# Performance work log

Hardware: AMD Instinct MI355X
Metric: run time of the kernel (lower is better)

The kernel has to match this reference:

```python
import jax, jax.numpy as jnp
import numpy as np

NUM_HEADS = 16

def setup_inputs() -> dict:
    key = jax.random.key(0)
    k1, k2, k3, k4, k5 = jax.random.split(key, 5)
    B, N, C = 4, 2048, 1024
    N2, Cy = 1024, 768
    x = jax.random.normal(k1, (B, N, C), dtype=jnp.float32)
    y = jax.random.normal(k2, (B, N2, Cy), dtype=jnp.float32)
    pad_mask = jax.random.randint(k3, (B, N), 0, 2).astype(jnp.bool_)
    # Linear weights (torch convention: out = inp @ W.T), scaled ~ fan-in init
    Wq = jax.random.normal(k4, (C, C), dtype=jnp.float32) * (C ** -0.5)
    Wkv = jax.random.normal(k5, (2 * C, Cy), dtype=jnp.float32) * (Cy ** -0.5)
    return {"x": x, "y": y, "pad_mask": pad_mask, "Wq": Wq, "Wkv": Wkv}


def reference(x, y, pad_mask, Wq, Wkv):
    B, N, C = x.shape
    N2 = y.shape[1]
    H = NUM_HEADS
    d = C // H
    scale = d ** -0.5
    # q: [B, H, N, d]
    q = (x @ Wq.T).reshape(B, N, H, d).transpose(0, 2, 1, 3)
    # kv: [B, N2, 2, H, d] -> k, v each [B, H, N2, d]
    kv = (y @ Wkv.T).reshape(B, N2, 2, H, d).transpose(2, 0, 3, 1, 4)
    k, v = kv[0], kv[1]
    # scores: [B, H, N, N2]
    attn = jnp.einsum("bhnd,bhmd->bhnm", q * scale, k)
    # pad_mask is indexed by the QUERY axis and broadcast over keys (faithful
    # to the original einops.repeat 'B Q -> B H Q L'). False -> -1e9.
    attn = jnp.where(pad_mask[:, None, :, None], attn, jnp.float32(-1e9))
    attn = jax.nn.softmax(attn, axis=-1)
    out = jnp.einsum("bhnm,bhmd->bhnd", attn, v)  # [B, H, N, d]
    return out.transpose(0, 2, 1, 3).reshape(B, N, C)
```

## Files before the change

kernel.cpp:

```cpp
#include <hip/hip_runtime.h>

typedef unsigned short u16;
typedef unsigned int u32;
typedef __attribute__((ext_vector_type(8))) __bf16 bf16x8;
typedef __attribute__((ext_vector_type(4))) float f32x4;

__device__ __forceinline__ u16 f2bf(float f) {
  unsigned u = __float_as_uint(f);
  u += 0x7FFFu + ((u >> 16) & 1u);
  return (u16)(u >> 16);
}

__device__ __forceinline__ float fast_exp2(float x) { return __builtin_amdgcn_exp2f(x); }
__device__ __forceinline__ float fast_rcp(float x) { return __builtin_amdgcn_rcpf(x); }

__global__ void cvt_all(const float* __restrict__ x, const float* __restrict__ Wq,
                        const float* __restrict__ y, const float* __restrict__ Wkv,
                        const int* __restrict__ mask,
                        u16* __restrict__ Xb, u16* __restrict__ Wqb,
                        u16* __restrict__ Yb, u16* __restrict__ Wkvb) {
  const int t = threadIdx.x;
  const int blk = blockIdx.x;
  const float4* src;
  u16* dst;
  int jb;
  float sc;
  bool m0 = false;
  if (blk < 2048) {
    src = (const float4*)x; dst = Xb; jb = blk * 1024 + t; m0 = true; sc = 1.0f;
  } else if (blk < 2304) {
    src = (const float4*)Wq; dst = Wqb; jb = (blk - 2048) * 1024 + t;
    sc = 0.18033688f;
  } else if (blk < 3072) {
    src = (const float4*)y; dst = Yb; jb = (blk - 2304) * 1024 + t; sc = 1.0f;
  } else {
    src = (const float4*)Wkv; dst = Wkvb; jb = (blk - 3072) * 1024 + t; sc = 1.0f;
  }
#pragma unroll
  for (int u = 0; u < 4; ++u) {
    const int j = jb + u * 256;
    float s = sc;
    if (m0) s = (mask[j >> 8] != 0) ? 1.0f : 0.0f;
    float4 v = src[j];
    ushort4 o;
    o.x = f2bf(v.x * s);
    o.y = f2bf(v.y * s);
    o.z = f2bf(v.z * s);
    o.w = f2bf(v.w * s);
    ((ushort4*)dst)[j] = o;
  }
}

__global__ __launch_bounds__(256) void gemm_dual(
    const u16* __restrict__ Aq, const u16* __restrict__ Bq, u16* __restrict__ Cq,
    const u16* __restrict__ Akv, const u16* __restrict__ Bkv, u16* __restrict__ Ckv,
    u16* __restrict__ Vt) {
  __shared__ __align__(16) u16 smem[17408];
  u16* sA = smem;
  u16* sB = smem + 8192;
  const int t = threadIdx.x;
  const int wave = t >> 6;
  const int lane = t & 63;
  const int wm = (wave >> 1) * 64;
  const int wn = (wave & 1) * 64;
  const int fr = lane & 15;
  const int quad = lane >> 4;
  const int fk = quad * 8;
  const int sr = lane >> 2;
  const int sc = (lane & 3) * 8;

  const u16 *A, *B;
  u16* C;
  int N, K, bx, by;
  const int blk = blockIdx.x;
  if (blk < 512) {
    A = Aq; B = Bq; C = Cq; N = 1024; K = 1024;
    by = blk >> 6; bx = blk & 63;
  } else {
    A = Akv; B = Bkv; C = Ckv; N = 2048; K = 768;
    const int id = blk - 512;
    by = id >> 5; bx = id & 31;
  }

  f32x4 acc[4][4];
  const f32x4 z4 = {0.f, 0.f, 0.f, 0.f};
#pragma unroll
  for (int i = 0; i < 4; ++i)
#pragma unroll
    for (int j = 0; j < 4; ++j) acc[i][j] = z4;

  const u16* Abase = A + (size_t)bx * 128 * K;
  const u16* Bbase = B + (size_t)by * 128 * K;

  auto stage = [&](int k0, u16* dA, u16* dB) {
#pragma unroll
    for (int q = 0; q < 2; ++q) {
      const int chunk = wave * 2 + q;
      const int row = chunk * 16 + sr;
      __builtin_amdgcn_global_load_lds(
          (__attribute__((address_space(1))) void*)(Abase + (size_t)row * K + k0 + sc),
          (__attribute__((address_space(3))) void*)(dA + chunk * 512), 16, 0, 0);
      __builtin_amdgcn_global_load_lds(
          (__attribute__((address_space(1))) void*)(Bbase + (size_t)row * K + k0 + sc),
          (__attribute__((address_space(3))) void*)(dB + chunk * 512), 16, 0, 0);
    }
  };

  stage(0, sA, sB);
  __syncthreads();

  int it = 0;
  for (int k0 = 0; k0 < K; k0 += 32, ++it) {
    u16* cA = sA + (it & 1) * 4096;
    u16* cB = sB + (it & 1) * 4096;
    if (k0 + 32 < K) stage(k0 + 32, sA + ((it + 1) & 1) * 4096, sB + ((it + 1) & 1) * 4096);

    bf16x8 af[4], bfv[4];
#pragma unroll
    for (int i = 0; i < 4; ++i)
      af[i] = *(const bf16x8*)(cA + (wm + i * 16 + fr) * 32 + fk);
#pragma unroll
    for (int j = 0; j < 4; ++j)
      bfv[j] = *(const bf16x8*)(cB + (wn + j * 16 + fr) * 32 + fk);
#pragma unroll
    for (int i = 0; i < 4; ++i)
#pragma unroll
      for (int j = 0; j < 4; ++j)
        acc[i][j] = __builtin_amdgcn_mfma_f32_16x16x32_bf16(af[i], bfv[j], acc[i][j], 0, 0, 0);

    if (k0 + 32 < K) __syncthreads();
  }

  if (blk >= 512 && by >= 8) {
    __syncthreads();
#pragma unroll
    for (int i = 0; i < 4; ++i)
#pragma unroll
      for (int j = 0; j < 4; ++j) {
        ushort4 o;
        o.x = f2bf(acc[i][j][0]);
        o.y = f2bf(acc[i][j][1]);
        o.z = f2bf(acc[i][j][2]);
        o.w = f2bf(acc[i][j][3]);
        *(ushort4*)(smem + (wn + j * 16 + fr) * 136 + wm + i * 16 + quad * 4) = o;
      }
    __syncthreads();
    const int b = bx >> 3;
#pragma unroll
    for (int i2 = 0; i2 < 32; ++i2) {
      const int flat = i2 * 256 + t;
      const int hdl = flat >> 6;
      const int pp = flat & 63;
      const int gg = pp >> 5;
      const int pe = (pp & 31) * 2;
      const int m = (pe & 32) | (pe & 3) | (((pe >> 3) & 3) << 2) | (((pe >> 2) & 1) << 4);
      const u32 val = *(const u32*)(smem + hdl * 136 + gg * 64 + m);
      const int h = (by - 8) * 2 + (hdl >> 6);
      const int dd = hdl & 63;
      *(u32*)(Vt + (size_t)((b * 16 + h) * 64 + dd) * 1024 +
              (bx & 7) * 128 + gg * 64 + pe) = val;
    }
  } else {
#pragma unroll
    for (int i = 0; i < 4; ++i)
#pragma unroll
      for (int j = 0; j < 4; ++j)
#pragma unroll
        for (int r = 0; r < 4; ++r) {
          const int row = bx * 128 + wm + i * 16 + quad * 4 + r;
          const int col = by * 128 + wn + j * 16 + fr;
          C[(size_t)row * N + col] = f2bf(acc[i][j][r]);
        }
  }
}

__global__ __launch_bounds__(256, 4) void attn_kernel(
    const u16* __restrict__ Q, const u16* __restrict__ KV,
    const u16* __restrict__ Vt, float* __restrict__ Out) {
  __shared__ __align__(16) u16 sK[2 * 64 * 64];
  __shared__ __align__(16) u16 sV[2 * 64 * 64];
  __shared__ float red[4][2][4][16];

  const int t = threadIdx.x;
  const int wave = t >> 6;
  const int lane = t & 63;
  const int g = blockIdx.x & 63;
  const int qt = blockIdx.x >> 6;
  const int b = g >> 4;
  const int h = g & 15;
  const int q0 = qt * 128;
  const int fr = lane & 15;
  const int quad = lane >> 4;
  const int l3 = lane >> 3, l7 = lane & 7;

  const u16* qbase = Q + (size_t)(b * 2048 + q0 + wave * 16 + fr) * 1024 + h * 64 + quad * 8;
  bf16x8 qa[2][2];
  qa[0][0] = *(const bf16x8*)(qbase);
  qa[0][1] = *(const bf16x8*)(qbase + 32);
  qa[1][0] = *(const bf16x8*)(qbase + (size_t)64 * 1024);
  qa[1][1] = *(const bf16x8*)(qbase + (size_t)64 * 1024 + 32);

  const int sq = (l7 ^ l3) * 8;
  auto stage = [&](int kcn, u16* dK, u16* dV) {
#pragma unroll
    for (int i = 0; i < 2; ++i) {
      const int j = wave * 2 + i;
      const u16* ksrc = KV + (size_t)(b * 1024 + kcn * 64 + 8 * j + l3) * 2048 + h * 64 + sq;
      __builtin_amdgcn_global_load_lds(
          (__attribute__((address_space(1))) void*)ksrc,
          (__attribute__((address_space(3))) void*)(dK + j * 512), 16, 0, 0);
      const u16* vsrc = Vt + (size_t)((b * 16 + h) * 64 + 8 * j + l3) * 1024 + kcn * 64 + sq;
      __builtin_amdgcn_global_load_lds(
          (__attribute__((address_space(1))) void*)vsrc,
          (__attribute__((address_space(3))) void*)(dV + j * 512), 16, 0, 0);
    }
  };

  stage(0, sK, sV);
  __syncthreads();

  const f32x4 z4 = {0.f, 0.f, 0.f, 0.f};
  f32x4 o[2][4];
  float l_run[2] = {0.f, 0.f};
#pragma unroll
  for (int hh = 0; hh < 2; ++hh)
#pragma unroll
    for (int nt = 0; nt < 4; ++nt) o[hh][nt] = z4;

  const int f7 = fr & 7;
  const int ck0 = (quad ^ f7) * 8;
  const int ck1 = ((quad ^ 4) ^ f7) * 8;

  for (int kc = 0; kc < 16; ++kc) {
    const u16* sKc = sK + (kc & 1) * 4096;
    const u16* sVc = sV + (kc & 1) * 4096;
    if (kc < 15) stage(kc + 1, sK + ((kc + 1) & 1) * 4096, sV + ((kc + 1) & 1) * 4096);

#pragma unroll
    for (int ks = 0; ks < 2; ++ks) {
      f32x4 s0[2], s1[2];
      {
        const u16* kb = sKc + ((2 * ks) * 16 + fr) * 64;
        bf16x8 k0 = *(const bf16x8*)(kb + ck0);
        bf16x8 k1 = *(const bf16x8*)(kb + ck1);
        s0[0] = __builtin_amdgcn_mfma_f32_16x16x32_bf16(k0, qa[0][0], z4, 0, 0, 0);
        s0[0] = __builtin_amdgcn_mfma_f32_16x16x32_bf16(k1, qa[0][1], s0[0], 0, 0, 0);
        s0[1] = __builtin_amdgcn_mfma_f32_16x16x32_bf16(k0, qa[1][0], z4, 0, 0, 0);
        s0[1] = __builtin_amdgcn_mfma_f32_16x16x32_bf16(k1, qa[1][1], s0[1], 0, 0, 0);
      }
      {
        const u16* kb = sKc + ((2 * ks + 1) * 16 + fr) * 64;
        bf16x8 k0 = *(const bf16x8*)(kb + ck0);
        bf16x8 k1 = *(const bf16x8*)(kb + ck1);
        s1[0] = __builtin_amdgcn_mfma_f32_16x16x32_bf16(k0, qa[0][0], z4, 0, 0, 0);
        s1[0] = __builtin_amdgcn_mfma_f32_16x16x32_bf16(k1, qa[0][1], s1[0], 0, 0, 0);
        s1[1] = __builtin_amdgcn_mfma_f32_16x16x32_bf16(k0, qa[1][0], z4, 0, 0, 0);
        s1[1] = __builtin_amdgcn_mfma_f32_16x16x32_bf16(k1, qa[1][1], s1[1], 0, 0, 0);
      }

      bf16x8 pa[2];
#pragma unroll
      for (int hh = 0; hh < 2; ++hh) {
        f32x4& a = (hh == 0) ? s0[0] : s0[1];
        f32x4& bb = (hh == 0) ? s1[0] : s1[1];
        float l = 0.f;
#pragma unroll
        for (int r = 0; r < 4; ++r) {
          float p0 = fast_exp2(a[r]); a[r] = p0; l += p0;
          float p1 = fast_exp2(bb[r]); bb[r] = p1; l += p1;
        }
        l_run[hh] += l;
        bf16x8 pv;
        pv[0] = (__bf16)a[0];  pv[1] = (__bf16)a[1];
        pv[2] = (__bf16)a[2];  pv[3] = (__bf16)a[3];
        pv[4] = (__bf16)bb[0]; pv[5] = (__bf16)bb[1];
        pv[6] = (__bf16)bb[2]; pv[7] = (__bf16)bb[3];
        pa[hh] = pv;
      }

#pragma unroll
      for (int ntd = 0; ntd < 4; ++ntd) {
        const int cv = (((ks * 4 + quad) ^ f7)) * 8;
        bf16x8 vb = *(const bf16x8*)(sVc + (ntd * 16 + fr) * 64 + cv);
        o[0][ntd] = __builtin_amdgcn_mfma_f32_16x16x32_bf16(pa[0], vb, o[0][ntd], 0, 0, 0);
        o[1][ntd] = __builtin_amdgcn_mfma_f32_16x16x32_bf16(pa[1], vb, o[1][ntd], 0, 0, 0);
      }
    }

    if (kc < 15) __syncthreads();
  }

  red[wave][0][quad][fr] = l_run[0];
  red[wave][1][quad][fr] = l_run[1];
  __syncthreads();

#pragma unroll
  for (int hh = 0; hh < 2; ++hh) {
    float inv[4];
#pragma unroll
    for (int r = 0; r < 4; ++r) {
      const int ql = quad * 4 + r;
      float d = red[wave][hh][0][ql] + red[wave][hh][1][ql] +
                red[wave][hh][2][ql] + red[wave][hh][3][ql];
      inv[r] = fast_rcp(d);
    }
#pragma unroll
    for (int ntd = 0; ntd < 4; ++ntd)
#pragma unroll
      for (int r = 0; r < 4; ++r) {
        const int row = q0 + hh * 64 + wave * 16 + quad * 4 + r;
        const int col = h * 64 + ntd * 16 + fr;
        Out[(size_t)(b * 2048 + row) * 1024 + col] = o[hh][ntd][r] * inv[r];
      }
  }
}

extern "C" void kernel_launch(void* const* d_in, const int* in_sizes, int n_in,
                              void* d_out, int out_size, void* d_ws, size_t ws_size,
                              hipStream_t stream) {
  (void)in_sizes; (void)n_in; (void)out_size; (void)ws_size;
  const float* x   = (const float*)d_in[0];
  const float* y   = (const float*)d_in[1];
  const int*   msk = (const int*)d_in[2];
  const float* Wq  = (const float*)d_in[3];
  const float* Wkv = (const float*)d_in[4];
  float* out = (float*)d_out;

  char* ws = (char*)d_ws;
  const size_t MB = 1024 * 1024;
  u16* Xb   = (u16*)(ws + 0);
  u16* Wqb  = (u16*)(ws + 16 * MB);
  u16* Yb   = (u16*)(ws + 18 * MB);
  u16* Wkvb = (u16*)(ws + 24 * MB);
  u16* Qb   = (u16*)(ws + 27 * MB);
  u16* KVb  = (u16*)(ws + 43 * MB);
  u16* Vtb  = (u16*)(ws + 59 * MB);

  cvt_all<<<3456, 256, 0, stream>>>(x, Wq, y, Wkv, msk, Xb, Wqb, Yb, Wkvb);
  gemm_dual<<<1024, 256, 0, stream>>>(Xb, Wqb, Qb, Yb, Wkvb, KVb, Vtb);
  attn_kernel<<<1024, 256, 0, stream>>>(Qb, KVb, Vtb, out);
}
```

Measured before the change: 180.1 us.

## Fuse fp32-to-bf16 activation conversion into projection GEMM and apply mask in epilogue

The conversion kernel now handles only the weights. The GEMM loads fp32 x and y directly into LDS with a XOR-swizzled layout and converts them to bf16 when it builds the MFMA fragments. The query pad mask moves from the activation conversion into the Q GEMM epilogue as a per-row scale. This drops the write and re-read of the bf16 activation copies, at the cost of twice the LDS traffic for A tiles and extra conversion instructions in the GEMM inner loop.

```diff
diff --git a/kernel.cpp b/kernel.cpp
--- a/kernel.cpp
+++ b/kernel.cpp
@@ -14,50 +14,37 @@
 __device__ __forceinline__ float fast_exp2(float x) { return __builtin_amdgcn_exp2f(x); }
 __device__ __forceinline__ float fast_rcp(float x) { return __builtin_amdgcn_rcpf(x); }
 
-__global__ void cvt_all(const float* __restrict__ x, const float* __restrict__ Wq,
-                        const float* __restrict__ y, const float* __restrict__ Wkv,
-                        const int* __restrict__ mask,
-                        u16* __restrict__ Xb, u16* __restrict__ Wqb,
-                        u16* __restrict__ Yb, u16* __restrict__ Wkvb) {
-  const int t = threadIdx.x;
-  const int blk = blockIdx.x;
+__global__ void cvt_w(const float* __restrict__ Wq, const float* __restrict__ Wkv,
+                      u16* __restrict__ Wqb, u16* __restrict__ Wkvb) {
+  int i = blockIdx.x * 256 + threadIdx.x;
   const float4* src;
   u16* dst;
-  int jb;
+  int j;
   float sc;
-  bool m0 = false;
-  if (blk < 2048) {
-    src = (const float4*)x; dst = Xb; jb = blk * 1024 + t; m0 = true; sc = 1.0f;
-  } else if (blk < 2304) {
-    src = (const float4*)Wq; dst = Wqb; jb = (blk - 2048) * 1024 + t;
+  if (i < 262144) {
+    src = (const float4*)Wq; dst = Wqb; j = i;
     sc = 0.18033688f;
-  } else if (blk < 3072) {
-    src = (const float4*)y; dst = Yb; jb = (blk - 2304) * 1024 + t; sc = 1.0f;
   } else {
-    src = (const float4*)Wkv; dst = Wkvb; jb = (blk - 3072) * 1024 + t; sc = 1.0f;
-  }
-#pragma unroll
-  for (int u = 0; u < 4; ++u) {
-    const int j = jb + u * 256;
-    float s = sc;
-    if (m0) s = (mask[j >> 8] != 0) ? 1.0f : 0.0f;
-    float4 v = src[j];
-    ushort4 o;
-    o.x = f2bf(v.x * s);
-    o.y = f2bf(v.y * s);
-    o.z = f2bf(v.z * s);
-    o.w = f2bf(v.w * s);
-    ((ushort4*)dst)[j] = o;
-  }
+    src = (const float4*)Wkv; dst = Wkvb; j = i - 262144; sc = 1.0f;
+  }
+  float4 v = src[j];
+  ushort4 o;
+  o.x = f2bf(v.x * sc);
+  o.y = f2bf(v.y * sc);
+  o.z = f2bf(v.z * sc);
+  o.w = f2bf(v.w * sc);
+  ((ushort4*)dst)[j] = o;
 }
 
 __global__ __launch_bounds__(256) void gemm_dual(
-    const u16* __restrict__ Aq, const u16* __restrict__ Bq, u16* __restrict__ Cq,
-    const u16* __restrict__ Akv, const u16* __restrict__ Bkv, u16* __restrict__ Ckv,
-    u16* __restrict__ Vt) {
-  __shared__ __align__(16) u16 smem[17408];
-  u16* sA = smem;
-  u16* sB = smem + 8192;
+    const float* __restrict__ Ax, const u16* __restrict__ Bq, u16* __restrict__ Cq,
+    const float* __restrict__ Ay, const u16* __restrict__ Bkv, u16* __restrict__ Ckv,
+    u16* __restrict__ Vt, const int* __restrict__ msk) {
+  __shared__ __align__(16) float smemf[12288];
+  float* sAf = smemf;
+  u16* sB = (u16*)(smemf + 8192);
+  u16* smem16 = (u16*)smemf;
+
   const int t = threadIdx.x;
   const int wave = t >> 6;
   const int lane = t & 63;
@@ -68,16 +55,18 @@
   const int fk = quad * 8;
   const int sr = lane >> 2;
   const int sc = (lane & 3) * 8;
-
-  const u16 *A, *B;
+  const int l3 = lane >> 3, l7 = lane & 7;
+
+  const float* A;
+  const u16* B;
   u16* C;
   int N, K, bx, by;
   const int blk = blockIdx.x;
   if (blk < 512) {
-    A = Aq; B = Bq; C = Cq; N = 1024; K = 1024;
+    A = Ax; B = Bq; C = Cq; N = 1024; K = 1024;
     by = blk >> 6; bx = blk & 63;
   } else {
-    A = Akv; B = Bkv; C = Ckv; N = 2048; K = 768;
+    A = Ay; B = Bkv; C = Ckv; N = 2048; K = 768;
     const int id = blk - 512;
     by = id >> 5; bx = id & 31;
   }
@@ -89,36 +78,50 @@
 #pragma unroll
     for (int j = 0; j < 4; ++j) acc[i][j] = z4;
 
-  const u16* Abase = A + (size_t)bx * 128 * K;
+  const float* Abase = A + (size_t)bx * 128 * K;
   const u16* Bbase = B + (size_t)by * 128 * K;
 
-  auto stage = [&](int k0, u16* dA, u16* dB) {
+  const int aCh = (l7 ^ l3) * 4;
+  auto stage = [&](int k0, float* dA, u16* dB) {
+#pragma unroll
+    for (int i = 0; i < 4; ++i) {
+      const int j = wave * 4 + i;
+      const float* asrc = Abase + (size_t)(8 * j + l3) * K + k0 + aCh;
+      __builtin_amdgcn_global_load_lds(
+          (__attribute__((address_space(1))) void*)asrc,
+          (__attribute__((address_space(3))) void*)(dA + j * 256), 16, 0, 0);
+    }
 #pragma unroll
     for (int q = 0; q < 2; ++q) {
       const int chunk = wave * 2 + q;
       const int row = chunk * 16 + sr;
       __builtin_amdgcn_global_load_lds(
-          (__attribute__((address_space(1))) void*)(Abase + (size_t)row * K + k0 + sc),
-          (__attribute__((address_space(3))) void*)(dA + chunk * 512), 16, 0, 0);
-      __builtin_amdgcn_global_load_lds(
           (__attribute__((address_space(1))) void*)(Bbase + (size_t)row * K + k0 + sc),
           (__attribute__((address_space(3))) void*)(dB + chunk * 512), 16, 0, 0);
     }
   };
 
-  stage(0, sA, sB);
+  stage(0, sAf, sB);
   __syncthreads();
 
+  const int f7 = fr & 7;
   int it = 0;
   for (int k0 = 0; k0 < K; k0 += 32, ++it) {
-    u16* cA = sA + (it & 1) * 4096;
-    u16* cB = sB + (it & 1) * 4096;
-    if (k0 + 32 < K) stage(k0 + 32, sA + ((it + 1) & 1) * 4096, sB + ((it + 1) & 1) * 4096);
+    const float* cA = sAf + (it & 1) * 4096;
+    const u16* cB = sB + (it & 1) * 4096;
+    if (k0 + 32 < K) stage(k0 + 32, sAf + ((it + 1) & 1) * 4096, sB + ((it + 1) & 1) * 4096);
 
     bf16x8 af[4], bfv[4];
 #pragma unroll
-    for (int i = 0; i < 4; ++i)
-      af[i] = *(const bf16x8*)(cA + (wm + i * 16 + fr) * 32 + fk);
+    for (int i = 0; i < 4; ++i) {
+      const int rb = (wm + i * 16 + fr) * 32;
+      float4 lo = *(const float4*)(cA + rb + (((2 * quad) ^ f7) * 4));
+      float4 hi = *(const float4*)(cA + rb + (((2 * quad + 1) ^ f7) * 4));
+      bf16x8 v;
+      v[0] = (__bf16)lo.x; v[1] = (__bf16)lo.y; v[2] = (__bf16)lo.z; v[3] = (__bf16)lo.w;
+      v[4] = (__bf16)hi.x; v[5] = (__bf16)hi.y; v[6] = (__bf16)hi.z; v[7] = (__bf16)hi.w;
+      af[i] = v;
+    }
 #pragma unroll
     for (int j = 0; j < 4; ++j)
       bfv[j] = *(const bf16x8*)(cB + (wn + j * 16 + fr) * 32 + fk);
@@ -142,7 +145,7 @@
         o.y = f2bf(acc[i][j][1]);
         o.z = f2bf(acc[i][j][2]);
         o.w = f2bf(acc[i][j][3]);
-        *(ushort4*)(smem + (wn + j * 16 + fr) * 136 + wm + i * 16 + quad * 4) = o;
+        *(ushort4*)(smem16 + (wn + j * 16 + fr) * 136 + wm + i * 16 + quad * 4) = o;
       }
     __syncthreads();
     const int b = bx >> 3;
@@ -154,23 +157,27 @@
       const int gg = pp >> 5;
       const int pe = (pp & 31) * 2;
       const int m = (pe & 32) | (pe & 3) | (((pe >> 3) & 3) << 2) | (((pe >> 2) & 1) << 4);
-      const u32 val = *(const u32*)(smem + hdl * 136 + gg * 64 + m);
+      const u32 val = *(const u32*)(smem16 + hdl * 136 + gg * 64 + m);
       const int h = (by - 8) * 2 + (hdl >> 6);
       const int dd = hdl & 63;
       *(u32*)(Vt + (size_t)((b * 16 + h) * 64 + dd) * 1024 +
               (bx & 7) * 128 + gg * 64 + pe) = val;
     }
   } else {
+    const bool isQ = (blk < 512);
 #pragma unroll
     for (int i = 0; i < 4; ++i)
 #pragma unroll
-      for (int j = 0; j < 4; ++j)
-#pragma unroll
-        for (int r = 0; r < 4; ++r) {
-          const int row = bx * 128 + wm + i * 16 + quad * 4 + r;
+      for (int r = 0; r < 4; ++r) {
+        const int row = bx * 128 + wm + i * 16 + quad * 4 + r;
+        float ms = 1.0f;
+        if (isQ) ms = (msk[row] != 0) ? 1.0f : 0.0f;
+#pragma unroll
+        for (int j = 0; j < 4; ++j) {
           const int col = by * 128 + wn + j * 16 + fr;
-          C[(size_t)row * N + col] = f2bf(acc[i][j][r]);
+          C[(size_t)row * N + col] = f2bf(acc[i][j][r] * ms);
         }
+      }
   }
 }
 
@@ -328,15 +335,13 @@
 
   char* ws = (char*)d_ws;
   const size_t MB = 1024 * 1024;
-  u16* Xb   = (u16*)(ws + 0);
-  u16* Wqb  = (u16*)(ws + 16 * MB);
-  u16* Yb   = (u16*)(ws + 18 * MB);
-  u16* Wkvb = (u16*)(ws + 24 * MB);
-  u16* Qb   = (u16*)(ws + 27 * MB);
-  u16* KVb  = (u16*)(ws + 43 * MB);
-  u16* Vtb  = (u16*)(ws + 59 * MB);
-
-  cvt_all<<<3456, 256, 0, stream>>>(x, Wq, y, Wkv, msk, Xb, Wqb, Yb, Wkvb);
-  gemm_dual<<<1024, 256, 0, stream>>>(Xb, Wqb, Qb, Yb, Wkvb, KVb, Vtb);
+  u16* Wqb  = (u16*)(ws + 0);
+  u16* Wkvb = (u16*)(ws + 2 * MB);
+  u16* Qb   = (u16*)(ws + 5 * MB);
+  u16* KVb  = (u16*)(ws + 21 * MB);
+  u16* Vtb  = (u16*)(ws + 37 * MB);
+
+  cvt_w<<<2560, 256, 0, stream>>>(Wq, Wkv, Wqb, Wkvb);
+  gemm_dual<<<1024, 256, 0, stream>>>(x, Wqb, Qb, y, Wkvb, KVb, Vtb, msk);
   attn_kernel<<<1024, 256, 0, stream>>>(Qb, KVb, Vtb, out);
 }
```

New measurement: 206.0 us. +14.4%, slower.
